# Optimization experiments

Hardware: AMD Instinct MI355X
Metric: run time of the kernel (lower is better)

The kernel has to match this reference:

```python
import jax, jax.numpy as jnp
import numpy as np

B, S, D = 2, 2048, 4096
H, KVH, HD = 32, 8, 128
MULT = 0.08838834764831845  # 1/sqrt(head_dim)
MAXV = 30.0                 # tanh soft-cap
ROPE_BASE = 10000.0


def _rope_cos_sin(position_ids, hd=HD, base=ROPE_BASE):
    inv_freq = 1.0 / (base ** (jnp.arange(0, hd, 2, dtype=jnp.float32) / hd))
    freqs = position_ids.astype(jnp.float32)[..., None] * inv_freq  # [B,S,hd/2]
    emb = jnp.concatenate([freqs, freqs], axis=-1)                  # [B,S,hd]
    return jnp.cos(emb), jnp.sin(emb)


def _rotate_half(x):
    half = x.shape[-1] // 2
    return jnp.concatenate([-x[..., half:], x[..., :half]], axis=-1)


def setup_inputs() -> dict:
    key = jax.random.key(0)
    ks = jax.random.split(key, 5)
    hidden_states = jax.random.normal(ks[0], (B, S, D), dtype=jnp.float32)
    position_ids = jnp.broadcast_to(jnp.arange(S, dtype=jnp.int64), (B, S))
    # True = masked (causal upper triangle)
    causal = jnp.triu(jnp.ones((S, S), dtype=bool), k=1)
    attention_mask = jnp.broadcast_to(causal, (B, 1, S, S))
    sc = 0.02
    q_w = jax.random.normal(ks[1], (D, H * HD), dtype=jnp.float32) * sc
    k_w = jax.random.normal(ks[2], (D, KVH * HD), dtype=jnp.float32) * sc
    v_w = jax.random.normal(ks[3], (D, KVH * HD), dtype=jnp.float32) * sc
    o_w = jax.random.normal(ks[4], (H * HD, D), dtype=jnp.float32) * sc
    return {"hidden_states": hidden_states, "position_ids": position_ids,
            "attention_mask": attention_mask, "q_w": q_w, "k_w": k_w,
            "v_w": v_w, "o_w": o_w}


def reference(hidden_states, position_ids, attention_mask, q_w, k_w, v_w, o_w):
    bsz, q_len, _ = hidden_states.shape
    q = (hidden_states @ q_w).reshape(bsz, q_len, H, HD).transpose(0, 2, 1, 3)    # [B,H,S,HD]
    k = (hidden_states @ k_w).reshape(bsz, q_len, KVH, HD).transpose(0, 2, 1, 3)  # [B,KVH,S,HD]
    v = (hidden_states @ v_w).reshape(bsz, q_len, KVH, HD).transpose(0, 2, 1, 3)

    cos, sin = _rope_cos_sin(position_ids)   # [B,S,HD]
    cos = cos[:, None]                       # [B,1,S,HD]
    sin = sin[:, None]
    q = q * cos + _rotate_half(q) * sin
    k = k * cos + _rotate_half(k) * sin

    groups = H // KVH
    k = jnp.repeat(k, groups, axis=1)        # [B,H,S,HD]
    v = jnp.repeat(v, groups, axis=1)

    scores = jnp.einsum('bhqd,bhkd->bhqk', q, k).astype(jnp.float32) * MULT
    scores = MAXV * jnp.tanh(scores / MAXV)
    scores = jnp.where(attention_mask, jnp.float32(-10000.0), scores)
    attn = jax.nn.softmax(scores, axis=-1).astype(q.dtype)

    out = jnp.einsum('bhqk,bhkd->bhqd', attn, v)       # [B,H,S,HD]
    out = out.transpose(0, 2, 1, 3).reshape(bsz, q_len, H * HD)
    return out @ o_w
```

## Files before the change

kernel.cpp:

```cpp
#include <hip/hip_runtime.h>
#include <stdint.h>

#define B_ 2
#define S_ 2048
#define D_ 4096
#define H_ 32
#define KVH_ 8
#define HD_ 128
#define GRP_ (H_/KVH_)
#define NQKV 6144
#define MULT_ 0.08838834764831845f
#define MAXV_ 30.0f

typedef __attribute__((ext_vector_type(8))) short s16x8;
typedef __attribute__((ext_vector_type(4))) float fx4;

__device__ __forceinline__ unsigned short f2bf(float f) {
  unsigned int u = __float_as_uint(f);
  u += 0x7fffu + ((u >> 16) & 1u);
  return (unsigned short)(u >> 16);
}
__device__ __forceinline__ float bf2f(unsigned short h) {
  return __uint_as_float(((unsigned int)h) << 16);
}
__device__ __forceinline__ uint32_t pk2(float lo, float hi) {
  return ((uint32_t)f2bf(hi) << 16) | (uint32_t)f2bf(lo);
}

__device__ __forceinline__ void gld_lds16(const void* g, void* l) {
  __builtin_amdgcn_global_load_lds(
      (const __attribute__((address_space(1))) unsigned int*)g,
      (__attribute__((address_space(3))) unsigned int*)l, 16, 0, 0);
}


__global__ void k_f2bf(const float* __restrict__ src, unsigned short* __restrict__ dst, int n4) {
  int i = blockIdx.x * blockDim.x + threadIdx.x;
  int stride = gridDim.x * blockDim.x;
  for (; i < n4; i += stride) {
    float4 v = ((const float4*)src)[i];
    ushort4 o;
    o.x = f2bf(v.x); o.y = f2bf(v.y); o.z = f2bf(v.z); o.w = f2bf(v.w);
    ((ushort4*)dst)[i] = o;
  }
}

__global__ void k_transpose_w(const float* __restrict__ src, int ncols,
                              unsigned short* __restrict__ dst) {
  __shared__ float tile[32][33];
  int k0 = blockIdx.x * 32;
  int n0 = blockIdx.y * 32;
  int tx = threadIdx.x, ty = threadIdx.y;
  for (int i = 0; i < 32; i += 8)
    tile[ty + i][tx] = src[(size_t)(k0 + ty + i) * ncols + n0 + tx];
  __syncthreads();
  for (int i = 0; i < 32; i += 8)
    dst[(size_t)(n0 + ty + i) * 4096 + k0 + tx] = f2bf(tile[tx][ty + i]);
}

__global__ void k_transpose_v(const unsigned short* __restrict__ qkv,
                              unsigned short* __restrict__ vt) {
  __shared__ unsigned short tile[32][33];
  int s0 = blockIdx.x * 32;
  int d0 = blockIdx.y * 32;
  int bk = blockIdx.z;
  int b = bk / KVH_, kvh = bk % KVH_;
  int tx = threadIdx.x, ty = threadIdx.y;
  for (int i = 0; i < 32; i += 8)
    tile[ty + i][tx] = qkv[(size_t)(b*S_ + s0 + ty + i)*NQKV + 5120 + kvh*HD_ + d0 + tx];
  __syncthreads();
  for (int i = 0; i < 32; i += 8)
    vt[((size_t)bk*HD_ + d0 + ty + i)*S_ + s0 + tx] = tile[tx][ty + i];
}

__global__ void k_rope(const unsigned short* __restrict__ qkv,
                       unsigned short* __restrict__ Q, unsigned short* __restrict__ K) {
  int bs = blockIdx.x;
  int b = bs >> 11;
  int s = bs & (S_ - 1);
  __shared__ float cs[64], sn[64];
  int t = threadIdx.x;
  if (t < 64) {
    float inv = __expf(-(float)t * 0.14391156831212787f);
    float fr = (float)s * inv;
    cs[t] = cosf(fr); sn[t] = sinf(fr);
  }
  __syncthreads();
  const unsigned short* row = qkv + (size_t)bs * NQKV;
  for (int i = t; i < H_*HD_; i += 256) {
    int h = i >> 7, d = i & 127;
    float x = bf2f(row[i]);
    float x2, c, si;
    if (d < 64) { x2 = -bf2f(row[h*128 + d + 64]); c = cs[d];    si = sn[d]; }
    else        { x2 =  bf2f(row[h*128 + d - 64]); c = cs[d-64]; si = sn[d-64]; }
    Q[((size_t)(b*H_ + h)*S_ + s)*HD_ + d] = f2bf(x*c + x2*si);
  }
  for (int i = t; i < KVH_*HD_; i += 256) {
    int h = i >> 7, d = i & 127;
    float x = bf2f(row[4096 + i]);
    float x2, c, si;
    if (d < 64) { x2 = -bf2f(row[4096 + h*128 + d + 64]); c = cs[d];    si = sn[d]; }
    else        { x2 =  bf2f(row[4096 + h*128 + d - 64]); c = cs[d-64]; si = sn[d-64]; }
    K[((size_t)(b*KVH_ + h)*S_ + s)*HD_ + d] = f2bf(x*c + x2*si);
  }
}


#define BAR() asm volatile("s_barrier" ::: "memory")
#define SB0() __builtin_amdgcn_sched_barrier(0)

#define STAGE(buf, isB, h, kt) do {                                          \
  const unsigned short* _src = (isB) ? Bt : A;                               \
  size_t _rb = (size_t)(((isB) ? bn : bm)*((isB) ? BN : 256)                 \
                        + (h)*((isB) ? BN/2 : 128));                         \
  _Pragma("unroll") for (int _rr = 0; _rr < ((isB) ? BN/128 : 2); ++_rr) {   \
    int _s = _rr*8 + wv;                                                     \
    gld_lds16(_src + (_rb + (size_t)((_s>>1)*16))*Kd                         \
                   + (size_t)((kt)*64 + (_s&1)*32) + lane_off,               \
              ldsc + (buf)*PBUF + (isB)*32768                                \
                   + (h)*((isB) ? BN*64 : 16384) + _s*1024);                 \
  }                                                                          \
} while (0)

#define LDA(dst, buf, mh) do {                                               \
  _Pragma("unroll") for (int _i = 0; _i < 4; ++_i)                           \
  _Pragma("unroll") for (int _kk = 0; _kk < 2; ++_kk)                        \
    dst[_i*2+_kk] = *(const s16x8*)(ldsc + (buf)*PBUF + wr*16384             \
                    + ((((mh)*4+_i)*2+_kk)*1024) + aswz);                    \
} while (0)

#define LDB(dst, buf, nh) do {                                               \
  _Pragma("unroll") for (int _j = 0; _j < NFR; ++_j)                         \
  _Pragma("unroll") for (int _kk = 0; _kk < 2; ++_kk)                        \
    dst[_j*2+_kk] = *(const s16x8*)(ldsc + (buf)*PBUF + 32768                \
                    + (wc>>1)*(BN*64)                                        \
                    + ((((wc&1)*2*NFR+(nh)*NFR+_j)*2+_kk)*1024) + aswz);     \
} while (0)

#define MFMA_Q(Aa, Bb, MH, NH) do {                                          \
  __builtin_amdgcn_s_setprio(1);                                            \
  _Pragma("unroll") for (int _i = 0; _i < 4; ++_i)                           \
  _Pragma("unroll") for (int _j = 0; _j < NFR; ++_j)                         \
  _Pragma("unroll") for (int _kk = 0; _kk < 2; ++_kk)                        \
    acc[(MH)*4+_i][(NH)*NFR+_j] = __builtin_amdgcn_mfma_f32_16x16x32_bf16(   \
        Aa[_i*2+_kk], Bb[_j*2+_kk], acc[(MH)*4+_i][(NH)*NFR+_j], 0, 0, 0);   \
  __builtin_amdgcn_s_setprio(0);                                            \
} while (0)

template<int OUTF32, int BN>
__global__ __launch_bounds__(512, 2)
void k_gemm8(const unsigned short* __restrict__ A, const unsigned short* __restrict__ Bt,
             void* __restrict__ C, int Kdim, int N, int MB) {
  constexpr int NFR = BN / 128;
  constexpr int PBUF = 32768 + BN * 128;
  __shared__ __align__(16) char ldsbuf[2 * PBUF];
  char* ldsc = ldsbuf;
  const size_t Kd = (size_t)Kdim;
  const int NT = Kdim >> 6;

  auto VMCN = [] {
    if constexpr (BN == 256) asm volatile("s_waitcnt vmcnt(4)" ::: "memory");
    else                     asm volatile("s_waitcnt vmcnt(2)" ::: "memory");
  };

  int nwg = gridDim.x;
  int flat = blockIdx.x;
  int q = nwg >> 3, r8 = nwg & 7, xcd = flat & 7, off = flat >> 3;
  int wg = (xcd < r8 ? xcd*(q+1) : r8*(q+1) + (xcd-r8)*q) + off;
  int bm = wg % MB, bn = wg / MB;

  int tid = threadIdx.x;
  int lane = tid & 63, wv = tid >> 6;
  int wr = wv >> 2, wc = wv & 3;
  int l15 = lane & 15, l4 = lane >> 4;
  const int aswz = (l15 << 6) + ((l4 << 4) ^ ((l15 & 8) ? 32 : 0));
  const size_t lane_off = (size_t)(lane >> 2) * Kd
                        + (size_t)(((lane & 3) << 3) ^ ((lane & 32) >> 1));

  fx4 acc[8][2*NFR] = {};
  s16x8 Afr[8], B0fr[2*NFR], B1fr[2*NFR];

  STAGE(0, 0, 0, 0); STAGE(0, 0, 1, 0);
  STAGE(0, 1, 0, 0); STAGE(0, 1, 1, 0);
  STAGE(1, 1, 0, 1); STAGE(1, 1, 1, 1);
  VMCN();
  BAR();

  for (int t2 = 0; t2 < NT; t2 += 2) {
    int tb1 = t2 + 1;
    int tn0 = t2 + 2; if (tn0 >= NT) tn0 -= NT;
    int tn1 = t2 + 3; if (tn1 >= NT) tn1 -= NT;
    LDA(Afr, 0, 0); LDB(B0fr, 0, 0);
    STAGE(1, 0, 0, tb1);
    BAR();
    MFMA_Q(Afr, B0fr, 0, 0);
    SB0(); BAR();
    LDB(B1fr, 0, 1);
    STAGE(1, 0, 1, tb1);
    BAR();
    MFMA_Q(Afr, B1fr, 0, 1);
    SB0(); BAR();
    LDA(Afr, 0, 1);
    STAGE(0, 1, 0, tn0);
    BAR();
    MFMA_Q(Afr, B1fr, 1, 1);
    SB0(); BAR();
    STAGE(0, 1, 1, tn0);
    BAR();
    MFMA_Q(Afr, B0fr, 1, 0);
    SB0(); VMCN(); BAR();
    LDA(Afr, 1, 0); LDB(B0fr, 1, 0);
    STAGE(0, 0, 0, tn0);
    BAR();
    MFMA_Q(Afr, B0fr, 0, 0);
    SB0(); BAR();
    LDB(B1fr, 1, 1);
    STAGE(0, 0, 1, tn0);
    BAR();
    MFMA_Q(Afr, B1fr, 0, 1);
    SB0(); BAR();
    LDA(Afr, 1, 1);
    STAGE(1, 1, 0, tn1);
    BAR();
    MFMA_Q(Afr, B1fr, 1, 1);
    SB0(); BAR();
    STAGE(1, 1, 1, tn1);
    BAR();
    MFMA_Q(Afr, B0fr, 1, 0);
    SB0(); VMCN(); BAR();
  }

  int m0 = bm*256 + wr*128 + l4*4;
#pragma unroll
  for (int mf = 0; mf < 8; ++mf)
#pragma unroll
    for (int nf = 0; nf < 2*NFR; ++nf)
#pragma unroll
      for (int r = 0; r < 4; ++r) {
        int m = m0 + mf*16 + r;
        int n = bn*BN + (wc>>1)*(BN/2) + ((wc&1)*2*NFR + nf)*16 + l15;
        float v = acc[mf][nf][r];
        if (OUTF32) ((float*)C)[(size_t)m*N + n] = v;
        else ((unsigned short*)C)[(size_t)m*N + n] = f2bf(v);
      }
}


__global__ __launch_bounds__(256)
void k_attn4(const unsigned short* __restrict__ Q, const unsigned short* __restrict__ K,
             const unsigned short* __restrict__ Vt, unsigned short* __restrict__ Aout) {
  const float C1 = 0.08838834764831845f * 2.0f * 1.4426950408889634f / 30.0f;
  const float C2 = 30.0f * 1.4426950408889634f;
  int fid = blockIdx.x;
  int xcd = fid & 7, idx = fid >> 3;
  int g = xcd*2 + (idx >> 5);
  int i = idx & 31;
  int tpair = i & 7, hlo = i >> 3;
  int b = g >> 3, kvh = g & 7;
  int h = kvh*GRP_ + hlo;
  int bh = b*H_ + h;
  int tid = threadIdx.x, lane = tid & 63, wv = tid >> 6;
  int l15 = lane & 15, l4 = lane >> 4;
  const unsigned short* Qb = Q + (size_t)bh * S_ * HD_;
  const unsigned short* Kb = K + (size_t)(b*KVH_ + kvh) * S_ * HD_;
  const unsigned short* Vb = Vt + (size_t)(b*KVH_ + kvh) * HD_ * S_;

  for (int sp = 0; sp < 2; ++sp) {
    int strip = sp ? (15 - tpair) : tpair;
    int q0 = strip * 128;
    int qbase = q0 + wv * 32;
    s16x8 bq[2][4];
#pragma unroll
    for (int qf = 0; qf < 2; ++qf)
#pragma unroll
      for (int kb = 0; kb < 4; ++kb)
        bq[qf][kb] = *(const s16x8*)&Qb[(size_t)(qbase + qf*16 + l15)*HD_ + kb*32 + l4*8];
    fx4 oacc[2][8] = {};
    float sump[2] = {0.f, 0.f};
    int nt = (qbase >> 5) + 1;
    for (int t = 0; t < nt; ++t) {
      int kbase = t*32;
      s16x8 kf[2][4];
#pragma unroll
      for (int nb = 0; nb < 2; ++nb)
#pragma unroll
        for (int kb = 0; kb < 4; ++kb)
          kf[nb][kb] = *(const s16x8*)&Kb[(size_t)(kbase + nb*16 + l15)*HD_ + kb*32 + l4*8];
      fx4 sst[2][2] = {};
#pragma unroll
      for (int nb = 0; nb < 2; ++nb)
#pragma unroll
        for (int kb = 0; kb < 4; ++kb) {
          sst[nb][0] = __builtin_amdgcn_mfma_f32_16x16x32_bf16(kf[nb][kb], bq[0][kb], sst[nb][0], 0, 0, 0);
          sst[nb][1] = __builtin_amdgcn_mfma_f32_16x16x32_bf16(kf[nb][kb], bq[1][kb], sst[nb][1], 0, 0, 0);
        }
      s16x8 pf[2];
#pragma unroll
      for (int qf = 0; qf < 2; ++qf) {
        int qr = qbase + qf*16 + l15;
        uint32_t w[4];
        float psum = 0.f;
#pragma unroll
        for (int nb = 0; nb < 2; ++nb) {
          float pv[4];
#pragma unroll
          for (int r = 0; r < 4; ++r) {
            int kk = kbase + nb*16 + l4*4 + r;
            float sraw = sst[nb][qf][r];
            float e2 = __builtin_amdgcn_exp2f(-fabsf(sraw) * C1);
            float th = (1.f - e2) * __builtin_amdgcn_rcpf(1.f + e2);
            float th_s = __uint_as_float(__float_as_uint(th) |
                                         (__float_as_uint(sraw) & 0x80000000u));
            float p = __builtin_amdgcn_exp2f(th_s * C2 - C2);
            p = (kk <= qr) ? p : 0.f;
            psum += p;
            pv[r] = p;
          }
          w[nb*2]   = pk2(pv[0], pv[1]);
          w[nb*2+1] = pk2(pv[2], pv[3]);
        }
        sump[qf] += psum;
        uint32_t a0x = __shfl_xor((int)w[0], 16), a1x = __shfl_xor((int)w[1], 16);
        uint32_t b0x = __shfl_xor((int)w[2], 16), b1x = __shfl_xor((int)w[3], 16);
        bool up = (l4 & 1);
        uint32_t VA0 = up ? a0x : w[0], VA1 = up ? a1x : w[1];
        uint32_t VA2 = up ? w[0] : a0x, VA3 = up ? w[1] : a1x;
        uint32_t VB0 = up ? b0x : w[2], VB1 = up ? b1x : w[3];
        uint32_t VB2 = up ? w[2] : b0x, VB3 = up ? w[3] : b1x;
        bool lowh = (l4 < 2);
        uint32_t X0 = lowh ? VB0 : VA0, X1 = lowh ? VB1 : VA1;
        uint32_t X2 = lowh ? VB2 : VA2, X3 = lowh ? VB3 : VA3;
        uint32_t Y0 = __shfl_xor((int)X0, 32), Y1 = __shfl_xor((int)X1, 32);
        uint32_t Y2 = __shfl_xor((int)X2, 32), Y3 = __shfl_xor((int)X3, 32);
        union { uint32_t u[4]; s16x8 v; } tw;
        tw.u[0] = (l4 == 0) ? VA0 : (l4 == 3) ? VB0 : Y0;
        tw.u[1] = (l4 == 0) ? VA1 : (l4 == 3) ? VB1 : Y1;
        tw.u[2] = (l4 == 0) ? VA2 : (l4 == 3) ? VB2 : Y2;
        tw.u[3] = (l4 == 0) ? VA3 : (l4 == 3) ? VB3 : Y3;
        pf[qf] = tw.v;
      }
#pragma unroll
      for (int db = 0; db < 8; ++db) {
        s16x8 vf = *(const s16x8*)&Vb[(size_t)(db*16 + l15)*S_ + kbase + l4*8];
        oacc[0][db] = __builtin_amdgcn_mfma_f32_16x16x32_bf16(vf, pf[0], oacc[0][db], 0, 0, 0);
        oacc[1][db] = __builtin_amdgcn_mfma_f32_16x16x32_bf16(vf, pf[1], oacc[1][db], 0, 0, 0);
      }
    }
#pragma unroll
    for (int qf = 0; qf < 2; ++qf) {
      float s = sump[qf];
      s += __shfl_xor(s, 16);
      s += __shfl_xor(s, 32);
      float rn = __builtin_amdgcn_rcpf(s);
      int qq = qbase + qf*16 + l15;
#pragma unroll
      for (int db = 0; db < 8; ++db) {
        ushort4 o;
        o.x = f2bf(oacc[qf][db][0] * rn);
        o.y = f2bf(oacc[qf][db][1] * rn);
        o.z = f2bf(oacc[qf][db][2] * rn);
        o.w = f2bf(oacc[qf][db][3] * rn);
        *(ushort4*)&Aout[(size_t)(b*S_ + qq)*4096 + h*HD_ + db*16 + l4*4] = o;
      }
    }
  }
}


extern "C" void kernel_launch(void* const* d_in, const int* in_sizes, int n_in,
                              void* d_out, int out_size, void* d_ws, size_t ws_size,
                              hipStream_t stream) {
  (void)in_sizes; (void)n_in; (void)out_size; (void)ws_size;
  const float* hidden = (const float*)d_in[0];
  const float* q_w = (const float*)d_in[3];
  const float* k_w = (const float*)d_in[4];
  const float* v_w = (const float*)d_in[5];
  const float* o_w = (const float*)d_in[6];
  char* ws = (char*)d_ws;
  unsigned short* hidden_bf = (unsigned short*)(ws + 0);
  unsigned short* qkv_wt    = (unsigned short*)(ws + 33554432);
  unsigned short* o_wt      = (unsigned short*)(ws + 83886080);
  unsigned short* qkv       = (unsigned short*)(ws + 117440512);
  unsigned short* Qb        = (unsigned short*)(ws + 167772160);
  unsigned short* Kb        = (unsigned short*)(ws + 201326592);
  unsigned short* Vt        = (unsigned short*)(ws + 209715200);
  unsigned short* attn_out  = (unsigned short*)(ws + 218103808);

  dim3 tb(32, 8);
  k_f2bf<<<2048, 256, 0, stream>>>(hidden, hidden_bf, (B_*S_*D_)/4);
  k_transpose_w<<<dim3(128, 128), tb, 0, stream>>>(q_w, 4096, qkv_wt);
  k_transpose_w<<<dim3(128, 32),  tb, 0, stream>>>(k_w, 1024, qkv_wt + (size_t)4096*4096);
  k_transpose_w<<<dim3(128, 32),  tb, 0, stream>>>(v_w, 1024, qkv_wt + (size_t)5120*4096);
  k_transpose_w<<<dim3(128, 128), tb, 0, stream>>>(o_w, 4096, o_wt);
  k_gemm8<0,128><<<dim3(16*48), 512, 0, stream>>>(hidden_bf, qkv_wt, qkv, D_, NQKV, 16);
  k_rope<<<B_*S_, 256, 0, stream>>>(qkv, Qb, Kb);
  k_transpose_v<<<dim3(S_/32, HD_/32, B_*KVH_), tb, 0, stream>>>(qkv, Vt);
  k_attn4<<<dim3(512), 256, 0, stream>>>(Qb, Kb, Vt, attn_out);
  k_gemm8<1,256><<<dim3(16*16), 512, 0, stream>>>(attn_out, o_wt, d_out, D_, D_, 16);
}
```

Baseline: 676.0 us.

## Stage K/V tiles in swizzled LDS and split attention grid per strip

The attention kernel now loads each 32-key K and V tile once per block into XOR-swizzled shared memory with direct global-to-LDS loads, so the four waves share it instead of each reading from global memory. The grid changes to one block per (query strip, head), with heavy strips launched first, and only the diagonal tile applies the causal mask. The row sum now comes from an extra MFMA against a ones vector, bf16 packing uses truncating byte permutes instead of rounding, and MFMA sections are wrapped with s_setprio. In exchange the kernel adds two block barriers per tile and gives up the previous XCD-aware mapping and pairing of light and heavy strips. Truncating P to bf16 also slightly changes numerics.

Measured after the change: 730.7 us. 8.1% more time.

```diff
diff --git a/kernel.cpp b/kernel.cpp
--- a/kernel.cpp
+++ b/kernel.cpp
@@ -22,9 +22,6 @@
 }
 __device__ __forceinline__ float bf2f(unsigned short h) {
   return __uint_as_float(((unsigned int)h) << 16);
-}
-__device__ __forceinline__ uint32_t pk2(float lo, float hi) {
-  return ((uint32_t)f2bf(hi) << 16) | (uint32_t)f2bf(lo);
 }
 
 __device__ __forceinline__ void gld_lds16(const void* g, void* l) {
@@ -246,122 +243,141 @@
 }
 
 
-__global__ __launch_bounds__(256)
-void k_attn4(const unsigned short* __restrict__ Q, const unsigned short* __restrict__ K,
+__global__ __launch_bounds__(256, 4)
+void k_attn6(const unsigned short* __restrict__ Q, const unsigned short* __restrict__ K,
              const unsigned short* __restrict__ Vt, unsigned short* __restrict__ Aout) {
+  __shared__ unsigned short k_lds[32*128];
+  __shared__ unsigned short v_lds[128*32];
   const float C1 = 0.08838834764831845f * 2.0f * 1.4426950408889634f / 30.0f;
   const float C2 = 30.0f * 1.4426950408889634f;
-  int fid = blockIdx.x;
-  int xcd = fid & 7, idx = fid >> 3;
-  int g = xcd*2 + (idx >> 5);
-  int i = idx & 31;
-  int tpair = i & 7, hlo = i >> 3;
-  int b = g >> 3, kvh = g & 7;
-  int h = kvh*GRP_ + hlo;
-  int bh = b*H_ + h;
+  int strip = 15 - blockIdx.x;
+  int bh = blockIdx.y;
+  int b = bh >> 5, h = bh & 31;
+  int kvh = h >> 2;
   int tid = threadIdx.x, lane = tid & 63, wv = tid >> 6;
   int l15 = lane & 15, l4 = lane >> 4;
   const unsigned short* Qb = Q + (size_t)bh * S_ * HD_;
   const unsigned short* Kb = K + (size_t)(b*KVH_ + kvh) * S_ * HD_;
   const unsigned short* Vb = Vt + (size_t)(b*KVH_ + kvh) * HD_ * S_;
 
-  for (int sp = 0; sp < 2; ++sp) {
-    int strip = sp ? (15 - tpair) : tpair;
-    int q0 = strip * 128;
-    int qbase = q0 + wv * 32;
-    s16x8 bq[2][4];
-#pragma unroll
-    for (int qf = 0; qf < 2; ++qf)
-#pragma unroll
-      for (int kb = 0; kb < 4; ++kb)
-        bq[qf][kb] = *(const s16x8*)&Qb[(size_t)(qbase + qf*16 + l15)*HD_ + kb*32 + l4*8];
-    fx4 oacc[2][8] = {};
-    float sump[2] = {0.f, 0.f};
-    int nt = (qbase >> 5) + 1;
-    for (int t = 0; t < nt; ++t) {
-      int kbase = t*32;
-      s16x8 kf[2][4];
-#pragma unroll
-      for (int nb = 0; nb < 2; ++nb)
-#pragma unroll
-        for (int kb = 0; kb < 4; ++kb)
-          kf[nb][kb] = *(const s16x8*)&Kb[(size_t)(kbase + nb*16 + l15)*HD_ + kb*32 + l4*8];
-      fx4 sst[2][2] = {};
-#pragma unroll
-      for (int nb = 0; nb < 2; ++nb)
-#pragma unroll
-        for (int kb = 0; kb < 4; ++kb) {
-          sst[nb][0] = __builtin_amdgcn_mfma_f32_16x16x32_bf16(kf[nb][kb], bq[0][kb], sst[nb][0], 0, 0, 0);
-          sst[nb][1] = __builtin_amdgcn_mfma_f32_16x16x32_bf16(kf[nb][kb], bq[1][kb], sst[nb][1], 0, 0, 0);
+  int q0 = strip * 128;
+  int qbase = q0 + wv * 32;
+  s16x8 bq[2][4];
+#pragma unroll
+  for (int qf = 0; qf < 2; ++qf)
+#pragma unroll
+    for (int kb = 0; kb < 4; ++kb)
+      bq[qf][kb] = *(const s16x8*)&Qb[(size_t)(qbase + qf*16 + l15)*HD_ + kb*32 + l4*8];
+
+  s16x8 ones;
+#pragma unroll
+  for (int i = 0; i < 8; ++i) ones[i] = (short)0x3F80;
+
+  fx4 oacc[2][8] = {};
+  fx4 osum[2] = {};
+
+  int nt_full = qbase >> 5;
+  int nt_blk = strip*4 + 4;
+
+  auto body = [&](int kbase, bool domask) {
+    fx4 sst[2][2] = {};
+    __builtin_amdgcn_s_setprio(1);
+#pragma unroll
+    for (int nb = 0; nb < 2; ++nb)
+#pragma unroll
+      for (int kb = 0; kb < 4; ++kb) {
+        s16x8 kf = *(const s16x8*)&k_lds[(nb*16 + l15)*128 + (((kb*4 + l4) ^ (l15 & 7)) * 8)];
+        sst[nb][0] = __builtin_amdgcn_mfma_f32_16x16x32_bf16(kf, bq[0][kb], sst[nb][0], 0, 0, 0);
+        sst[nb][1] = __builtin_amdgcn_mfma_f32_16x16x32_bf16(kf, bq[1][kb], sst[nb][1], 0, 0, 0);
+      }
+    __builtin_amdgcn_s_setprio(0);
+    s16x8 pf[2];
+#pragma unroll
+    for (int qf = 0; qf < 2; ++qf) {
+      int qr = qbase + qf*16 + l15;
+      uint32_t w[4];
+#pragma unroll
+      for (int nb = 0; nb < 2; ++nb) {
+        float pv[4];
+#pragma unroll
+        for (int r = 0; r < 4; ++r) {
+          float sraw = sst[nb][qf][r];
+          float e2 = __builtin_amdgcn_exp2f(-fabsf(sraw) * C1);
+          float th = (1.f - e2) * __builtin_amdgcn_rcpf(1.f + e2);
+          float th_s = __uint_as_float(__float_as_uint(th) |
+                                       (__float_as_uint(sraw) & 0x80000000u));
+          float p = __builtin_amdgcn_exp2f(th_s * C2 - C2);
+          if (domask) {
+            int kk = kbase + nb*16 + l4*4 + r;
+            p = (kk <= qr) ? p : 0.f;
+          }
+          pv[r] = p;
         }
-      s16x8 pf[2];
-#pragma unroll
-      for (int qf = 0; qf < 2; ++qf) {
-        int qr = qbase + qf*16 + l15;
-        uint32_t w[4];
-        float psum = 0.f;
-#pragma unroll
-        for (int nb = 0; nb < 2; ++nb) {
-          float pv[4];
-#pragma unroll
-          for (int r = 0; r < 4; ++r) {
-            int kk = kbase + nb*16 + l4*4 + r;
-            float sraw = sst[nb][qf][r];
-            float e2 = __builtin_amdgcn_exp2f(-fabsf(sraw) * C1);
-            float th = (1.f - e2) * __builtin_amdgcn_rcpf(1.f + e2);
-            float th_s = __uint_as_float(__float_as_uint(th) |
-                                         (__float_as_uint(sraw) & 0x80000000u));
-            float p = __builtin_amdgcn_exp2f(th_s * C2 - C2);
-            p = (kk <= qr) ? p : 0.f;
-            psum += p;
-            pv[r] = p;
-          }
-          w[nb*2]   = pk2(pv[0], pv[1]);
-          w[nb*2+1] = pk2(pv[2], pv[3]);
-        }
-        sump[qf] += psum;
-        uint32_t a0x = __shfl_xor((int)w[0], 16), a1x = __shfl_xor((int)w[1], 16);
-        uint32_t b0x = __shfl_xor((int)w[2], 16), b1x = __shfl_xor((int)w[3], 16);
-        bool up = (l4 & 1);
-        uint32_t VA0 = up ? a0x : w[0], VA1 = up ? a1x : w[1];
-        uint32_t VA2 = up ? w[0] : a0x, VA3 = up ? w[1] : a1x;
-        uint32_t VB0 = up ? b0x : w[2], VB1 = up ? b1x : w[3];
-        uint32_t VB2 = up ? w[2] : b0x, VB3 = up ? w[3] : b1x;
-        bool lowh = (l4 < 2);
-        uint32_t X0 = lowh ? VB0 : VA0, X1 = lowh ? VB1 : VA1;
-        uint32_t X2 = lowh ? VB2 : VA2, X3 = lowh ? VB3 : VA3;
-        uint32_t Y0 = __shfl_xor((int)X0, 32), Y1 = __shfl_xor((int)X1, 32);
-        uint32_t Y2 = __shfl_xor((int)X2, 32), Y3 = __shfl_xor((int)X3, 32);
-        union { uint32_t u[4]; s16x8 v; } tw;
-        tw.u[0] = (l4 == 0) ? VA0 : (l4 == 3) ? VB0 : Y0;
-        tw.u[1] = (l4 == 0) ? VA1 : (l4 == 3) ? VB1 : Y1;
-        tw.u[2] = (l4 == 0) ? VA2 : (l4 == 3) ? VB2 : Y2;
-        tw.u[3] = (l4 == 0) ? VA3 : (l4 == 3) ? VB3 : Y3;
-        pf[qf] = tw.v;
+        w[nb*2]   = __builtin_amdgcn_perm(__float_as_uint(pv[1]), __float_as_uint(pv[0]), 0x07060302u);
+        w[nb*2+1] = __builtin_amdgcn_perm(__float_as_uint(pv[3]), __float_as_uint(pv[2]), 0x07060302u);
       }
-#pragma unroll
-      for (int db = 0; db < 8; ++db) {
-        s16x8 vf = *(const s16x8*)&Vb[(size_t)(db*16 + l15)*S_ + kbase + l4*8];
-        oacc[0][db] = __builtin_amdgcn_mfma_f32_16x16x32_bf16(vf, pf[0], oacc[0][db], 0, 0, 0);
-        oacc[1][db] = __builtin_amdgcn_mfma_f32_16x16x32_bf16(vf, pf[1], oacc[1][db], 0, 0, 0);
-      }
+      uint32_t a0x = __shfl_xor((int)w[0], 16), a1x = __shfl_xor((int)w[1], 16);
+      uint32_t b0x = __shfl_xor((int)w[2], 16), b1x = __shfl_xor((int)w[3], 16);
+      bool up = (l4 & 1);
+      uint32_t VA0 = up ? a0x : w[0], VA1 = up ? a1x : w[1];
+      uint32_t VA2 = up ? w[0] : a0x, VA3 = up ? w[1] : a1x;
+      uint32_t VB0 = up ? b0x : w[2], VB1 = up ? b1x : w[3];
+      uint32_t VB2 = up ? w[2] : b0x, VB3 = up ? w[3] : b1x;
+      bool lowh = (l4 < 2);
+      uint32_t X0 = lowh ? VB0 : VA0, X1 = lowh ? VB1 : VA1;
+      uint32_t X2 = lowh ? VB2 : VA2, X3 = lowh ? VB3 : VA3;
+      uint32_t Y0 = __shfl_xor((int)X0, 32), Y1 = __shfl_xor((int)X1, 32);
+      uint32_t Y2 = __shfl_xor((int)X2, 32), Y3 = __shfl_xor((int)X3, 32);
+      union { uint32_t u[4]; s16x8 v; } tw;
+      tw.u[0] = (l4 == 0) ? VA0 : (l4 == 3) ? VB0 : Y0;
+      tw.u[1] = (l4 == 0) ? VA1 : (l4 == 3) ? VB1 : Y1;
+      tw.u[2] = (l4 == 0) ? VA2 : (l4 == 3) ? VB2 : Y2;
+      tw.u[3] = (l4 == 0) ? VA3 : (l4 == 3) ? VB3 : Y3;
+      pf[qf] = tw.v;
     }
-#pragma unroll
-    for (int qf = 0; qf < 2; ++qf) {
-      float s = sump[qf];
-      s += __shfl_xor(s, 16);
-      s += __shfl_xor(s, 32);
-      float rn = __builtin_amdgcn_rcpf(s);
-      int qq = qbase + qf*16 + l15;
-#pragma unroll
-      for (int db = 0; db < 8; ++db) {
-        ushort4 o;
-        o.x = f2bf(oacc[qf][db][0] * rn);
-        o.y = f2bf(oacc[qf][db][1] * rn);
-        o.z = f2bf(oacc[qf][db][2] * rn);
-        o.w = f2bf(oacc[qf][db][3] * rn);
-        *(ushort4*)&Aout[(size_t)(b*S_ + qq)*4096 + h*HD_ + db*16 + l4*4] = o;
-      }
+    __builtin_amdgcn_s_setprio(1);
+    osum[0] = __builtin_amdgcn_mfma_f32_16x16x32_bf16(ones, pf[0], osum[0], 0, 0, 0);
+    osum[1] = __builtin_amdgcn_mfma_f32_16x16x32_bf16(ones, pf[1], osum[1], 0, 0, 0);
+#pragma unroll
+    for (int db = 0; db < 8; ++db) {
+      int d = db*16 + l15;
+      s16x8 vf = *(const s16x8*)&v_lds[d*32 + ((l4 ^ (d & 3)) * 8)];
+      oacc[0][db] = __builtin_amdgcn_mfma_f32_16x16x32_bf16(vf, pf[0], oacc[0][db], 0, 0, 0);
+      oacc[1][db] = __builtin_amdgcn_mfma_f32_16x16x32_bf16(vf, pf[1], oacc[1][db], 0, 0, 0);
+    }
+    __builtin_amdgcn_s_setprio(0);
+  };
+
+  for (int t = 0; t < nt_blk; ++t) {
+    int kbase = t*32;
+#pragma unroll
+    for (int it = 0; it < 2; ++it) {
+      int c = it*256 + tid;
+      int kr = c >> 4;
+      int kd = ((c & 15) ^ (kr & 7)) * 8;
+      gld_lds16(&Kb[(size_t)(kbase + kr)*HD_ + kd], &k_lds[it*2048 + wv*512]);
+      int vd = c >> 2;
+      int vk = ((c & 3) ^ (vd & 3)) * 8;
+      gld_lds16(&Vb[(size_t)vd*S_ + kbase + vk], &v_lds[it*2048 + wv*512]);
+    }
+    __syncthreads();
+    if (t < nt_full)       body(kbase, false);
+    else if (t == nt_full) body(kbase, true);
+    __syncthreads();
+  }
+
+#pragma unroll
+  for (int qf = 0; qf < 2; ++qf) {
+    float rn = __builtin_amdgcn_rcpf(osum[qf][0]);
+    int qq = qbase + qf*16 + l15;
+#pragma unroll
+    for (int db = 0; db < 8; ++db) {
+      ushort4 o;
+      o.x = f2bf(oacc[qf][db][0] * rn);
+      o.y = f2bf(oacc[qf][db][1] * rn);
+      o.z = f2bf(oacc[qf][db][2] * rn);
+      o.w = f2bf(oacc[qf][db][3] * rn);
+      *(ushort4*)&Aout[(size_t)(b*S_ + qq)*4096 + h*HD_ + db*16 + l4*4] = o;
     }
   }
 }
@@ -395,6 +411,6 @@
   k_gemm8<0,128><<<dim3(16*48), 512, 0, stream>>>(hidden_bf, qkv_wt, qkv, D_, NQKV, 16);
   k_rope<<<B_*S_, 256, 0, stream>>>(qkv, Qb, Kb);
   k_transpose_v<<<dim3(S_/32, HD_/32, B_*KVH_), tb, 0, stream>>>(qkv, Vt);
-  k_attn4<<<dim3(512), 256, 0, stream>>>(Qb, Kb, Vt, attn_out);
+  k_attn6<<<dim3(16, 64), 256, 0, stream>>>(Qb, Kb, Vt, attn_out);
   k_gemm8<1,256><<<dim3(16*16), 512, 0, stream>>>(attn_out, o_wt, d_out, D_, D_, 16);
 }
```
